# Performance work log

Measured on AMD Instinct MI355X. Metric: run time of the kernel, lower is better.

Reference implementation:

```python
import jax, jax.numpy as jnp
import numpy as np

B, L, E, H = 4, 2048, 1024, 16
D = E // H  # head_dim = 64


def setup_inputs() -> dict:
    key = jax.random.key(0)
    ks = jax.random.split(key, 8)
    s = 0.02
    return {
        "queries": jax.random.normal(ks[0], (B, L, E), jnp.float32),
        "keys": jax.random.normal(ks[1], (B, L, E), jnp.float32),
        "values": jax.random.normal(ks[2], (B, L, E), jnp.float32),
        "mask": jnp.ones((B, 1, L, L), jnp.int32),
        "Wq": jax.random.normal(ks[3], (E, E), jnp.float32) * s,
        "Wk": jax.random.normal(ks[4], (E, E), jnp.float32) * s,
        "Wv": jax.random.normal(ks[5], (E, E), jnp.float32) * s,
        "Wo": jax.random.normal(ks[6], (E, E), jnp.float32) * s,
        "bo": jax.random.normal(ks[7], (E,), jnp.float32) * s,
    }


def reference(queries, keys, values, mask, Wq, Wk, Wv, Wo, bo):
    # Linear projections (torch Linear: x @ W.T)
    q = (queries @ Wq.T).reshape(B, -1, H, D)
    k = (keys @ Wk.T).reshape(B, -1, H, D)
    v = (values @ Wv.T).reshape(B, -1, H, D)
    # scores: [B, H, Lq, Lk]
    scores = jnp.einsum("bqhd,bkhd->bhqk", q, k)
    # masked_fill BEFORE scaling, exactly as the original
    scores = jnp.where(mask == 0, jnp.float32(-1e20), scores)
    attn = jax.nn.softmax(scores / jnp.sqrt(jnp.float32(E)), axis=3)
    out = jnp.einsum("bhql,blhd->bqhd", attn, v).reshape(B, -1, H * D)
    return out @ Wo.T + bo
```

## Files before the change

kernel.cpp:

```cpp
#include <hip/hip_runtime.h>
#include <hip/hip_bf16.h>

#define B_ 4
#define L_ 2048
#define E_ 1024
#define H_ 16
#define D_ 64
#define KDIM 1024

typedef unsigned short u16;
typedef unsigned short u16x8 __attribute__((ext_vector_type(8)));
typedef short s16x8 __attribute__((ext_vector_type(8)));
typedef short s16x4 __attribute__((ext_vector_type(4)));
typedef float f32x4 __attribute__((ext_vector_type(4)));
typedef unsigned uint2v __attribute__((ext_vector_type(2)));

#define MFMA32(a, b, c) __builtin_amdgcn_mfma_f32_16x16x32_bf16(a, b, c, 0, 0, 0)

#if __has_builtin(__builtin_amdgcn_mfma_f32_16x16x16bf16_1k)
#define HAVE_M16 1
#define MFMA16(a, b, c) __builtin_amdgcn_mfma_f32_16x16x16bf16_1k(a, b, c, 0, 0, 0)
#else
#define HAVE_M16 0
#endif

__device__ inline u16 f2bf(float f) {
  union { float f; unsigned u; } v; v.f = f;
  unsigned r = v.u + 0x7fffu + ((v.u >> 16) & 1u);
  return (u16)(r >> 16);
}
__device__ inline float bf2f(u16 h) {
  union { unsigned u; float f; } v; v.u = ((unsigned)h) << 16;
  return v.f;
}
__device__ inline unsigned permrne(float hi, float lo) {
  unsigned a = __float_as_uint(lo) + 0x8000u;
  unsigned b = __float_as_uint(hi) + 0x8000u;
  return __builtin_amdgcn_perm(b, a, 0x07060302u);
}
__device__ inline float bperm_f(int byteaddr, float v) {
  return __uint_as_float((unsigned)__builtin_amdgcn_ds_bpermute(byteaddr, (int)__float_as_uint(v)));
}

typedef __attribute__((address_space(1))) const unsigned as1_u32;
typedef __attribute__((address_space(3))) unsigned as3_u32;
__device__ inline void gl_lds16(const u16* g, u16* l) {
  __builtin_amdgcn_global_load_lds((as1_u32*)g, (as3_u32*)l, 16, 0, 0);
}

__global__ __launch_bounds__(256) void detect_k(const u16* __restrict__ q, int* __restrict__ flag) {
  int tid = threadIdx.x;
  int cnt = 0;
  for (int i = tid; i < 4096; i += 256) {
    unsigned e = (q[i] >> 7) & 0xFFu;
    if (e >= 0xC0u) cnt++;
  }
  __shared__ int s[256];
  s[tid] = cnt;
  __syncthreads();
  for (int off = 128; off; off >>= 1) {
    if (tid < off) s[tid] += s[tid + off];
    __syncthreads();
  }
  if (tid == 0) *flag = (s[0] >= 16) ? 1 : 0;
}

__global__ __launch_bounds__(256) void mask_bits_k(const int* __restrict__ mask,
                                                   unsigned long long* __restrict__ bits,
                                                   unsigned* __restrict__ gflag, int words) {
  int gw = (int)((blockIdx.x * 256 + threadIdx.x) >> 6);
  int lane = threadIdx.x & 63;
  if (gw >= words) return;
  int mv = mask[(size_t)gw * 64 + lane];
  unsigned long long bal = __ballot(mv != 0);
  if (lane == 0) {
    bits[gw] = bal;
    if (bal != ~0ULL) atomicAnd(gflag, 0u);
  }
}

__global__ __launch_bounds__(256) void cvt_bf16_k(const void* __restrict__ src, u16* __restrict__ dst,
                                                  int n8, const int* __restrict__ flagp) {
  int i = blockIdx.x * 256 + threadIdx.x;
  if (i >= n8) return;
  if (*flagp) {
    const float* s = (const float*)src + (size_t)i * 8;
    f32x4 a = *(const f32x4*)s;
    f32x4 b = *(const f32x4*)(s + 4);
    u16x8 o;
#pragma unroll
    for (int j = 0; j < 4; ++j) { o[j] = f2bf(a[j]); o[4 + j] = f2bf(b[j]); }
    *((u16x8*)dst + i) = o;
  } else {
    *((u16x8*)dst + i) = *((const u16x8*)src + i);
  }
}
__global__ __launch_bounds__(256) void cvt_f32_k(const void* __restrict__ src, float* __restrict__ dst,
                                                 int n, const int* __restrict__ flagp) {
  int i = blockIdx.x * 256 + threadIdx.x;
  if (i >= n) return;
  dst[i] = (*flagp) ? ((const float*)src)[i] : bf2f(((const u16*)src)[i]);
}

__device__ inline void gemm_core(const u16* __restrict__ A, const u16* __restrict__ W,
                                 int m0, int n0, u16* AsB, u16* BsB, f32x4 (&acc)[4][4]) {
  const int tid = threadIdx.x;
  const int wave = tid >> 6, lane = tid & 63;
  const int quad = lane >> 4, l16 = lane & 15;
  const int wm = wave >> 1, wn = wave & 1;
  const int lrow = lane >> 3;
  const int lch = (lane & 7) ^ lrow;

#pragma unroll
  for (int i = 0; i < 4; ++i)
#pragma unroll
    for (int j = 0; j < 4; ++j)
#pragma unroll
      for (int u = 0; u < 4; ++u) acc[i][j][u] = 0.f;

  const u16* gA = A + (size_t)(m0 + wave * 32 + lrow) * KDIM + lch * 8;
  const u16* gB = W + (size_t)(n0 + wave * 32 + lrow) * KDIM + lch * 8;

  for (int k0 = 0; k0 < KDIM; k0 += 64) {
    __syncthreads();
#pragma unroll
    for (int i = 0; i < 4; ++i) {
      gl_lds16(gA + (size_t)i * 8 * KDIM + k0, &AsB[(wave * 32 + i * 8) * 64]);
      gl_lds16(gB + (size_t)i * 8 * KDIM + k0, &BsB[(wave * 32 + i * 8) * 64]);
    }
    __syncthreads();
#pragma unroll
    for (int ks = 0; ks < 2; ++ks) {
      s16x8 af[4], bf[4];
#pragma unroll
      for (int mt = 0; mt < 4; ++mt) {
        int row = wm * 64 + mt * 16 + l16;
        af[mt] = *(const s16x8*)&AsB[row * 64 + (((quad + 4 * ks) ^ (row & 7)) * 8)];
      }
#pragma unroll
      for (int nt = 0; nt < 4; ++nt) {
        int row = wn * 64 + nt * 16 + l16;
        bf[nt] = *(const s16x8*)&BsB[row * 64 + (((quad + 4 * ks) ^ (row & 7)) * 8)];
      }
#pragma unroll
      for (int mt = 0; mt < 4; ++mt)
#pragma unroll
        for (int nt = 0; nt < 4; ++nt)
          acc[mt][nt] = MFMA32(af[mt], bf[nt], acc[mt][nt]);
    }
  }
}

#define SCALE_Q 0.045084220f
#define MASKC  -4.508422e18f

__global__ __launch_bounds__(256) void gemm_qk_k(
    const void* __restrict__ qor, const void* __restrict__ kor,
    const void* __restrict__ wqor, const void* __restrict__ wkor,
    const u16* __restrict__ qc, const u16* __restrict__ kc,
    const u16* __restrict__ wqc, const u16* __restrict__ wkc,
    u16* __restrict__ Qp, u16* __restrict__ Kp, const int* __restrict__ flagp) {
  const int isf32 = *flagp;
  const int z = blockIdx.z;
  const u16* A = z ? (isf32 ? kc : (const u16*)kor) : (isf32 ? qc : (const u16*)qor);
  const u16* W = z ? (isf32 ? wkc : (const u16*)wkor) : (isf32 ? wqc : (const u16*)wqor);
  u16* C = z ? Kp : Qp;
  const float scale = z ? 1.0f : SCALE_Q;
  __shared__ __align__(16) u16 As[128 * 64];
  __shared__ __align__(16) u16 Bs[128 * 64];
  f32x4 acc[4][4];
  const int m0 = blockIdx.y * 128, n0 = blockIdx.x * 128;
  gemm_core(A, W, m0, n0, As, Bs, acc);

  const int lane = threadIdx.x & 63, wave = threadIdx.x >> 6;
  const int quad = lane >> 4, l16 = lane & 15;
  const int wm = wave >> 1, wn = wave & 1;
#pragma unroll
  for (int mt = 0; mt < 4; ++mt)
#pragma unroll
    for (int r = 0; r < 4; ++r) {
      int row = m0 + wm * 64 + mt * 16 + quad * 4 + r;
      int bb = row >> 11, l = row & (L_ - 1);
#pragma unroll
      for (int nt = 0; nt < 4; ++nt) {
        int col = n0 + wn * 64 + nt * 16 + l16;
        int hh = col >> 6, d = col & 63;
        C[(((size_t)bb * H_ + hh) * L_ + l) * D_ + d] = f2bf(acc[mt][nt][r] * scale);
      }
    }
}

__global__ __launch_bounds__(256) void gemm_vt_k(
    const void* __restrict__ vor, const void* __restrict__ wvor,
    const u16* __restrict__ vc, const u16* __restrict__ wvc,
    u16* __restrict__ VpT, const int* __restrict__ flagp) {
  const int isf32 = *flagp;
  const u16* A = isf32 ? wvc : (const u16*)wvor;
  const u16* W = isf32 ? vc : (const u16*)vor;
  __shared__ __align__(16) u16 As[128 * 64];
  __shared__ __align__(16) u16 Bs[128 * 64];
  f32x4 acc[4][4];
  const int m0 = blockIdx.y * 128, n0 = blockIdx.x * 128;
  gemm_core(A, W, m0, n0, As, Bs, acc);

  const int lane = threadIdx.x & 63, wave = threadIdx.x >> 6;
  const int quad = lane >> 4, l16 = lane & 15;
  const int wm = wave >> 1, wn = wave & 1;
#pragma unroll
  for (int mt = 0; mt < 4; ++mt)
#pragma unroll
    for (int r = 0; r < 4; ++r) {
      int o = m0 + wm * 64 + mt * 16 + quad * 4 + r;
      int hh = o >> 6, d = o & 63;
#pragma unroll
      for (int nt = 0; nt < 4; ++nt) {
        int t = n0 + wn * 64 + nt * 16 + l16;
        int bb = t >> 11, l = t & (L_ - 1);
        VpT[(((size_t)bb * H_ + hh) * D_ + d) * L_ + l] = f2bf(acc[mt][nt][r]);
      }
    }
}

__global__ __launch_bounds__(256) void gemm_out_k(
    const u16* __restrict__ AO, const void* __restrict__ woor, const u16* __restrict__ woc,
    const float* __restrict__ bo_f, void* __restrict__ outp, const int* __restrict__ flagp) {
  const int isf32 = *flagp;
  const u16* A = AO;
  const u16* W = isf32 ? woc : (const u16*)woor;
  __shared__ __align__(16) u16 As[128 * 64];
  __shared__ __align__(16) u16 Bs[128 * 64];
  f32x4 acc[4][4];
  const int m0 = blockIdx.y * 128, n0 = blockIdx.x * 128;
  gemm_core(A, W, m0, n0, As, Bs, acc);

  const int lane = threadIdx.x & 63, wave = threadIdx.x >> 6;
  const int quad = lane >> 4, l16 = lane & 15;
  const int wm = wave >> 1, wn = wave & 1;
#pragma unroll
  for (int mt = 0; mt < 4; ++mt)
#pragma unroll
    for (int r = 0; r < 4; ++r) {
      int row = m0 + wm * 64 + mt * 16 + quad * 4 + r;
#pragma unroll
      for (int nt = 0; nt < 4; ++nt) {
        int col = n0 + wn * 64 + nt * 16 + l16;
        float v = acc[mt][nt][r] + bo_f[col];
        if (isf32) ((float*)outp)[(size_t)row * E_ + col] = v;
        else ((u16*)outp)[(size_t)row * E_ + col] = f2bf(v);
      }
    }
}

__global__ __launch_bounds__(256) void attn_st(
    const u16* __restrict__ Qp, const u16* __restrict__ Kp, const u16* __restrict__ VpT,
    const unsigned long long* __restrict__ Mb, const unsigned* __restrict__ allonesp,
    u16* __restrict__ AO) {
  const int qt = blockIdx.x, h = blockIdx.y, b = blockIdx.z;
  const int tid = threadIdx.x;
  const int wave = tid >> 6, lane = tid & 63;
  const int quad = lane >> 4, l16 = lane & 15;
  const size_t bh = ((size_t)b * H_ + h) * (size_t)(L_ * D_);
  const int q0w = qt * 64 + wave * 16;
  const bool aone = (*allonesp) != 0u;

  __shared__ __align__(16) u16 Ks[64 * 64];
  __shared__ __align__(16) u16 Vs[64 * 64];
#if !HAVE_M16
  __shared__ __align__(16) u16 Ps[4][16 * 72];
#endif

  s16x8 bq[2];
  {
    const u16* qp = &Qp[bh + (size_t)(q0w + l16) * D_ + quad * 8];
    bq[0] = *(const s16x8*)qp;
    bq[1] = *(const s16x8*)(qp + 32);
  }

  f32x4 Oacc[4];
#pragma unroll
  for (int nt = 0; nt < 4; ++nt)
#pragma unroll
    for (int u = 0; u < 4; ++u) Oacc[nt][u] = 0.f;
  float m_i = -3.0e38f, l_i = 0.f;

  const int lrow = lane >> 3, lch = (lane & 7) ^ lrow;

  for (int kt = 0; kt < L_ / 64; ++kt) {
    const int k0 = kt * 64;
    __syncthreads();
#pragma unroll
    for (int i = 0; i < 2; ++i) {
      int row = wave * 16 + i * 8 + lrow;
      gl_lds16(&Kp[bh + (size_t)(k0 + row) * D_ + lch * 8], &Ks[(wave * 16 + i * 8) * 64]);
      gl_lds16(&VpT[bh + (size_t)row * L_ + k0 + lch * 8], &Vs[(wave * 16 + i * 8) * 64]);
    }
    __syncthreads();

    f32x4 st[4];
#pragma unroll
    for (int nt = 0; nt < 4; ++nt) {
#pragma unroll
      for (int u = 0; u < 4; ++u) st[nt][u] = 0.f;
#pragma unroll
      for (int ks = 0; ks < 2; ++ks) {
        int row = nt * 16 + l16;
        s16x8 ak = *(const s16x8*)&Ks[row * 64 + (((quad + 4 * ks) ^ (row & 7)) * 8)];
        st[nt] = MFMA32(ak, bq[ks], st[nt]);
      }
    }

    float sv[4][4];
    if (aone) {
#pragma unroll
      for (int nt = 0; nt < 4; ++nt)
#pragma unroll
        for (int r = 0; r < 4; ++r) sv[nt][r] = st[nt][r];
    } else {
      unsigned long long mb = Mb[((size_t)b * L_ + q0w + l16) * (L_ / 64) + kt];
      unsigned long long mq = mb >> (quad * 4);
#pragma unroll
      for (int nt = 0; nt < 4; ++nt)
#pragma unroll
        for (int r = 0; r < 4; ++r)
          sv[nt][r] = ((mq >> (nt * 16 + r)) & 1ULL) ? st[nt][r] : MASKC;
    }

    float mx = sv[0][0];
#pragma unroll
    for (int nt = 0; nt < 4; ++nt)
#pragma unroll
      for (int r = 0; r < 4; ++r) mx = fmaxf(mx, sv[nt][r]);
    mx = fmaxf(mx, __shfl_xor(mx, 16));
    mx = fmaxf(mx, __shfl_xor(mx, 32));
    float newm = fmaxf(m_i, mx);
    float alpha = exp2f(m_i - newm);

    float p[4][4];
    float rs = 0.f;
#pragma unroll
    for (int nt = 0; nt < 4; ++nt)
#pragma unroll
      for (int r = 0; r < 4; ++r) {
        float e = exp2f(sv[nt][r] - newm);
        p[nt][r] = e;
        rs += e;
      }
    rs += __shfl_xor(rs, 16);
    rs += __shfl_xor(rs, 32);
    l_i = l_i * alpha + rs;
    m_i = newm;

#pragma unroll
    for (int r = 0; r < 4; ++r) {
      float aO = bperm_f((quad * 4 + r) * 4, alpha);
      Oacc[0][r] *= aO; Oacc[1][r] *= aO; Oacc[2][r] *= aO; Oacc[3][r] *= aO;
    }

#if HAVE_M16
#pragma unroll
    for (int knt = 0; knt < 4; ++knt) {
      unsigned pk0 = permrne(p[knt][1], p[knt][0]);
      unsigned pk1 = permrne(p[knt][3], p[knt][2]);
      union { uint2v u; s16x4 v; } pa;
      pa.u[0] = pk0; pa.u[1] = pk1;
      const int kkb = knt * 16 + quad * 4;
      const int kch = kkb >> 3, kin = kkb & 7;
#pragma unroll
      for (int nt = 0; nt < 4; ++nt) {
        int row = nt * 16 + l16;
        s16x4 vb = *(const s16x4*)&Vs[row * 64 + ((kch ^ (row & 7)) * 8) + kin];
        Oacc[nt] = MFMA16(pa.v, vb, Oacc[nt]);
      }
    }
#else
#pragma unroll
    for (int nt = 0; nt < 4; ++nt) {
      uint2v w;
      w[0] = permrne(p[nt][1], p[nt][0]);
      w[1] = permrne(p[nt][3], p[nt][2]);
      *(uint2v*)&Ps[wave][l16 * 72 + nt * 16 + quad * 4] = w;
    }
#pragma unroll
    for (int ks = 0; ks < 2; ++ks) {
      s16x8 pa = *(const s16x8*)&Ps[wave][l16 * 72 + quad * 8 + 32 * ks];
#pragma unroll
      for (int nt = 0; nt < 4; ++nt) {
        int row = nt * 16 + l16;
        s16x8 vb = *(const s16x8*)&Vs[row * 64 + (((quad + 4 * ks) ^ (row & 7)) * 8)];
        Oacc[nt] = MFMA32(pa, vb, Oacc[nt]);
      }
    }
#endif
  }

#pragma unroll
  for (int r = 0; r < 4; ++r) {
    float lr = bperm_f((quad * 4 + r) * 4, l_i);
    float inv = 1.0f / lr;
    int row = q0w + quad * 4 + r;
#pragma unroll
    for (int nt = 0; nt < 4; ++nt) {
      int col = h * 64 + nt * 16 + l16;
      AO[((size_t)b * L_ + row) * E_ + col] = f2bf(Oacc[nt][r] * inv);
    }
  }
}

__device__ inline u16x8 load8_cvt(const void* base, size_t elem_off, int isf32) {
  if (isf32) {
    const float* p = (const float*)base + elem_off;
    f32x4 lo = *(const f32x4*)p;
    f32x4 hi = *(const f32x4*)(p + 4);
    u16x8 t;
#pragma unroll
    for (int j = 0; j < 4; ++j) { t[j] = f2bf(lo[j]); t[4 + j] = f2bf(hi[j]); }
    return t;
  } else {
    return *((const u16x8*)base + elem_off / 8);
  }
}

template <int QKV>
__global__ __launch_bounds__(256) void gemm128(
    const void* __restrict__ A0, const void* __restrict__ A1, const void* __restrict__ A2,
    const void* __restrict__ W0, const void* __restrict__ W1, const void* __restrict__ W2,
    const void* __restrict__ bias,
    void* __restrict__ C0, u16* __restrict__ C1, u16* __restrict__ C2,
    int M, int N, int Kd, const int* __restrict__ flagp) {
  const void* A = A0; const void* W = W0; void* C = C0;
  if (QKV) {
    if (blockIdx.z == 1) { A = A1; W = W1; C = C1; }
    else if (blockIdx.z == 2) { A = A2; W = W2; C = C2; }
  }
  const int isf32 = *flagp;
  const int aF32 = QKV ? isf32 : 0;
  const int tid = threadIdx.x;
  const int wave = tid >> 6, lane = tid & 63;
  const int quad = lane >> 4, l16 = lane & 15;
  const int wm = wave >> 1, wn = wave & 1;
  const int m0 = blockIdx.y * 128, n0 = blockIdx.x * 128;
  __shared__ u16 As[128 * 32];
  __shared__ u16 Bs[128 * 32];
  f32x4 acc[4][4];
#pragma unroll
  for (int i = 0; i < 4; ++i)
#pragma unroll
    for (int j = 0; j < 4; ++j)
#pragma unroll
      for (int u = 0; u < 4; ++u) acc[i][j][u] = 0.f;
  const int row_s = tid >> 2;
  const int cb_s = tid & 3;
  for (int k0 = 0; k0 < Kd; k0 += 32) {
    __syncthreads();
#pragma unroll
    for (int rr = 0; rr < 2; ++rr) {
      int row = rr * 64 + row_s;
      int sw = (cb_s ^ ((row >> 1) & 3)) * 8;
      *(u16x8*)&As[row * 32 + sw] = load8_cvt(A, (size_t)(m0 + row) * Kd + k0 + cb_s * 8, aF32);
      *(u16x8*)&Bs[row * 32 + sw] = load8_cvt(W, (size_t)(n0 + row) * Kd + k0 + cb_s * 8, isf32);
    }
    __syncthreads();
    s16x8 af[4], bfv[4];
#pragma unroll
    for (int mt = 0; mt < 4; ++mt) {
      int row = wm * 64 + mt * 16 + l16;
      af[mt] = *(const s16x8*)&As[row * 32 + (quad ^ ((row >> 1) & 3)) * 8];
    }
#pragma unroll
    for (int nt = 0; nt < 4; ++nt) {
      int row = wn * 64 + nt * 16 + l16;
      bfv[nt] = *(const s16x8*)&Bs[row * 32 + (quad ^ ((row >> 1) & 3)) * 8];
    }
#pragma unroll
    for (int mt = 0; mt < 4; ++mt)
#pragma unroll
      for (int nt = 0; nt < 4; ++nt)
        acc[mt][nt] = MFMA32(af[mt], bfv[nt], acc[mt][nt]);
  }
#pragma unroll
  for (int mt = 0; mt < 4; ++mt)
#pragma unroll
    for (int r = 0; r < 4; ++r) {
      int row = m0 + wm * 64 + mt * 16 + quad * 4 + r;
#pragma unroll
      for (int nt = 0; nt < 4; ++nt) {
        int col = n0 + wn * 64 + nt * 16 + l16;
        float v = acc[mt][nt][r];
        if (!QKV) {
          v += isf32 ? ((const float*)bias)[col] : bf2f(((const u16*)bias)[col]);
          if (isf32) ((float*)C)[(size_t)row * N + col] = v;
          else ((u16*)C)[(size_t)row * N + col] = f2bf(v);
        } else {
          int bb = row >> 11, l = row & (L_ - 1);
          int hh = col >> 6, d = col & 63;
          ((u16*)C)[(((size_t)bb * H_ + hh) * L_ + l) * D_ + d] = f2bf(v);
        }
      }
    }
}

__global__ __launch_bounds__(256) void attn64(const u16* __restrict__ Qp, const u16* __restrict__ Kp,
                                              const u16* __restrict__ Vp,
                                              const unsigned long long* __restrict__ Mb,
                                              u16* __restrict__ AO) {
  const int qt = blockIdx.x, h = blockIdx.y, b = blockIdx.z;
  const int tid = threadIdx.x;
  const int wave = tid >> 6, lane = tid & 63;
  const int quad = lane >> 4, l16 = lane & 15;
  const size_t bh = ((size_t)b * H_ + h) * (size_t)(L_ * D_);
  const int q0 = qt * 64;
  __shared__ u16 Ksl[64 * 72];
  __shared__ u16 Vtl[64 * 72];
  __shared__ u16 Psl[4][16 * 72];
  s16x8 aq[2];
  {
    int qrow = q0 + wave * 16 + l16;
#pragma unroll
    for (int ks = 0; ks < 2; ++ks)
      aq[ks] = *(const s16x8*)&Qp[bh + (size_t)qrow * D_ + quad * 8 + 32 * ks];
  }
  f32x4 Oacc[4];
#pragma unroll
  for (int nt = 0; nt < 4; ++nt)
#pragma unroll
    for (int u = 0; u < 4; ++u) Oacc[nt][u] = 0.f;
  float m_i[4], l_i[4];
#pragma unroll
  for (int r = 0; r < 4; ++r) { m_i[r] = -3.0e38f; l_i[r] = 0.f; }
  const float invs = 0.03125f;
  const float LOG2E = 1.44269504088896f;
  for (int kt = 0; kt < L_ / 64; ++kt) {
    const int k0 = kt * 64;
    __syncthreads();
#pragma unroll
    for (int rr = 0; rr < 2; ++rr) {
      int row = rr * 32 + (tid >> 3);
      int col = (tid & 7) * 8;
      *(u16x8*)&Ksl[row * 72 + col] = *(const u16x8*)&Kp[bh + (size_t)(k0 + row) * D_ + col];
    }
    {
      int d0 = wave * 16;
#pragma unroll
      for (int half = 0; half < 2; ++half) {
        u16x8 tv = *(const u16x8*)&Vp[bh + (size_t)(k0 + lane) * D_ + d0 + half * 8];
#pragma unroll
        for (int j = 0; j < 8; ++j) Vtl[(d0 + half * 8 + j) * 72 + lane] = tv[j];
      }
    }
    __syncthreads();
    f32x4 sacc[4];
#pragma unroll
    for (int nt = 0; nt < 4; ++nt) {
#pragma unroll
      for (int u = 0; u < 4; ++u) sacc[nt][u] = 0.f;
#pragma unroll
      for (int ks = 0; ks < 2; ++ks) {
        s16x8 bfr = *(const s16x8*)&Ksl[(nt * 16 + l16) * 72 + quad * 8 + 32 * ks];
        sacc[nt] = MFMA32(aq[ks], bfr, sacc[nt]);
      }
    }
    float sv[4][4], alph[4];
#pragma unroll
    for (int r = 0; r < 4; ++r) {
      int row = q0 + wave * 16 + quad * 4 + r;
      unsigned long long mb = Mb[(size_t)(b * L_ + row) * (L_ / 64) + kt];
#pragma unroll
      for (int nt = 0; nt < 4; ++nt) {
        float s = sacc[nt][r] * invs;
        if (!((mb >> (nt * 16 + l16)) & 1ULL)) s = -3.125e18f;
        sv[nt][r] = s;
      }
      float mx = fmaxf(fmaxf(sv[0][r], sv[1][r]), fmaxf(sv[2][r], sv[3][r]));
      mx = fmaxf(mx, __shfl_xor(mx, 1));
      mx = fmaxf(mx, __shfl_xor(mx, 2));
      mx = fmaxf(mx, __shfl_xor(mx, 4));
      mx = fmaxf(mx, __shfl_xor(mx, 8));
      float newm = fmaxf(m_i[r], mx);
      float alpha = exp2f((m_i[r] - newm) * LOG2E);
      float rs = 0.f;
#pragma unroll
      for (int nt = 0; nt < 4; ++nt) {
        float pp = exp2f((sv[nt][r] - newm) * LOG2E);
        rs += pp;
        Psl[wave][(quad * 4 + r) * 72 + nt * 16 + l16] = f2bf(pp);
      }
      rs += __shfl_xor(rs, 1);
      rs += __shfl_xor(rs, 2);
      rs += __shfl_xor(rs, 4);
      rs += __shfl_xor(rs, 8);
      l_i[r] = l_i[r] * alpha + rs;
      m_i[r] = newm;
      alph[r] = alpha;
    }
#pragma unroll
    for (int nt = 0; nt < 4; ++nt)
#pragma unroll
      for (int r = 0; r < 4; ++r) Oacc[nt][r] *= alph[r];
#pragma unroll
    for (int ks = 0; ks < 2; ++ks) {
      s16x8 pa = *(const s16x8*)&Psl[wave][l16 * 72 + quad * 8 + 32 * ks];
#pragma unroll
      for (int nt = 0; nt < 4; ++nt) {
        s16x8 vb = *(const s16x8*)&Vtl[(nt * 16 + l16) * 72 + quad * 8 + 32 * ks];
        Oacc[nt] = MFMA32(pa, vb, Oacc[nt]);
      }
    }
  }
#pragma unroll
  for (int nt = 0; nt < 4; ++nt)
#pragma unroll
    for (int r = 0; r < 4; ++r) {
      int row = q0 + wave * 16 + quad * 4 + r;
      int col = h * 64 + nt * 16 + l16;
      AO[((size_t)b * L_ + row) * E_ + col] = f2bf(Oacc[nt][r] / l_i[r]);
    }
}

extern "C" void kernel_launch(void* const* d_in, const int* in_sizes, int n_in,
                              void* d_out, int out_size, void* d_ws, size_t ws_size,
                              hipStream_t stream) {
  const void* queries = d_in[0];
  const void* keys = d_in[1];
  const void* values = d_in[2];
  const int* mask = (const int*)d_in[3];
  const void* Wq = d_in[4];
  const void* Wk = d_in[5];
  const void* Wv = d_in[6];
  const void* Wo = d_in[7];
  const void* bo = d_in[8];

  char* ws = (char*)d_ws;
  const int words = B_ * L_ * (L_ / 64);
  const size_t NEED = 111153408;

  if (ws_size >= NEED) {
    const size_t SZQ = (size_t)B_ * L_ * E_ * 2;
    const size_t SZW = (size_t)E_ * E_ * 2;
    u16* qc = (u16*)(ws + 0);
    u16* kc = (u16*)(ws + SZQ);
    u16* vc = (u16*)(ws + 2 * SZQ);
    u16* wqc = (u16*)(ws + 3 * SZQ);
    u16* wkc = (u16*)(ws + 3 * SZQ + SZW);
    u16* wvc = (u16*)(ws + 3 * SZQ + 2 * SZW);
    u16* woc = (u16*)(ws + 3 * SZQ + 3 * SZW);
    float* bo_f = (float*)(ws + 3 * SZQ + 4 * SZW);
    char* p2 = ws + 3 * SZQ + 4 * SZW + 4096;
    u16* Qp = (u16*)(p2);
    u16* Kp = (u16*)(p2 + SZQ);
    u16* VpT = (u16*)(p2 + 2 * SZQ);
    unsigned long long* Mb = (unsigned long long*)(p2 + 3 * SZQ);
    char* pf = p2 + 3 * SZQ + (size_t)words * 8;
    int* flag = (int*)pf;
    unsigned* gflag = (unsigned*)(pf + 4);
    u16* AO = qc;

    hipLaunchKernelGGL(detect_k, dim3(1), dim3(256), 0, stream, (const u16*)queries, flag);
    hipMemsetAsync(gflag, 1, 4, stream);
    hipLaunchKernelGGL(mask_bits_k, dim3(words / 4), dim3(256), 0, stream, mask, Mb, gflag, words);

    int n8q = (B_ * L_ * E_) / 8, n8w = (E_ * E_) / 8;
    hipLaunchKernelGGL(cvt_bf16_k, dim3(n8q / 256), dim3(256), 0, stream, queries, qc, n8q, flag);
    hipLaunchKernelGGL(cvt_bf16_k, dim3(n8q / 256), dim3(256), 0, stream, keys, kc, n8q, flag);
    hipLaunchKernelGGL(cvt_bf16_k, dim3(n8q / 256), dim3(256), 0, stream, values, vc, n8q, flag);
    hipLaunchKernelGGL(cvt_bf16_k, dim3(n8w / 256), dim3(256), 0, stream, Wq, wqc, n8w, flag);
    hipLaunchKernelGGL(cvt_bf16_k, dim3(n8w / 256), dim3(256), 0, stream, Wk, wkc, n8w, flag);
    hipLaunchKernelGGL(cvt_bf16_k, dim3(n8w / 256), dim3(256), 0, stream, Wv, wvc, n8w, flag);
    hipLaunchKernelGGL(cvt_bf16_k, dim3(n8w / 256), dim3(256), 0, stream, Wo, woc, n8w, flag);
    hipLaunchKernelGGL(cvt_f32_k, dim3(E_ / 256), dim3(256), 0, stream, bo, bo_f, E_, flag);

    hipLaunchKernelGGL(gemm_qk_k, dim3(E_ / 128, (B_ * L_) / 128, 2), dim3(256), 0, stream,
                       queries, keys, Wq, Wk, qc, kc, wqc, wkc, Qp, Kp, flag);
    hipLaunchKernelGGL(gemm_vt_k, dim3((B_ * L_) / 128, E_ / 128, 1), dim3(256), 0, stream,
                       values, Wv, vc, wvc, VpT, flag);
    hipLaunchKernelGGL(attn_st, dim3(L_ / 64, H_, B_), dim3(256), 0, stream,
                       Qp, Kp, VpT, Mb, gflag, AO);
    hipLaunchKernelGGL(gemm_out_k, dim3(E_ / 128, (B_ * L_) / 128, 1), dim3(256), 0, stream,
                       AO, Wo, woc, bo_f, d_out, flag);
  } else {
    const size_t SEG = (size_t)B_ * H_ * L_ * D_ * sizeof(u16);
    u16* Qp = (u16*)(ws);
    u16* Kp = (u16*)(ws + SEG);
    u16* Vp = (u16*)(ws + 2 * SEG);
    u16* AO = (u16*)(ws + 3 * SEG);
    int* flag = (int*)(ws + 4 * SEG);
    unsigned* gflag = (unsigned*)(ws + 4 * SEG + 8);
    unsigned long long* Mb = (unsigned long long*)(ws + 4 * SEG + 256);

    hipLaunchKernelGGL(detect_k, dim3(1), dim3(256), 0, stream, (const u16*)queries, flag);
    hipMemsetAsync(gflag, 1, 4, stream);
    hipLaunchKernelGGL(mask_bits_k, dim3(words / 4), dim3(256), 0, stream, mask, Mb, gflag, words);
    dim3 g1(E_ / 128, (B_ * L_) / 128, 3);
    hipLaunchKernelGGL((gemm128<1>), g1, dim3(256), 0, stream,
                       queries, keys, values, Wq, Wk, Wv, (const void*)nullptr,
                       (void*)Qp, Kp, Vp, B_ * L_, E_, E_, flag);
    hipLaunchKernelGGL(attn64, dim3(L_ / 64, H_, B_), dim3(256), 0, stream, Qp, Kp, Vp, Mb, AO);
    dim3 g2(E_ / 128, (B_ * L_) / 128, 1);
    hipLaunchKernelGGL((gemm128<0>), g2, dim3(256), 0, stream,
                       (const void*)AO, (const void*)nullptr, (const void*)nullptr,
                       Wo, (const void*)nullptr, (const void*)nullptr, bo,
                       d_out, (u16*)nullptr, (u16*)nullptr, B_ * L_, E_, E_, flag);
  }
}
```

Before: 486.3 us.

## Fuse conversion and projection launches, widen attention K tile to 128 with fp16 PV

Merges the eight per-tensor conversion launches into one kernel, and the Q/K and V projection GEMMs into a single three-slice launch. V is now stored in fp16. The attention kernel processes 128 keys per iteration with a new swizzled V layout and uses fp16 MFMA for P·V, with probabilities packed by cvt_pkrtz and raw exp2 intrinsics. The aims are to cut launch overhead and halve the number of attention loop iterations and syncs. The costs are more LDS and registers per block and fp16 range and precision for V and P.

```diff
diff --git a/kernel.cpp b/kernel.cpp
--- a/kernel.cpp
+++ b/kernel.cpp
@@ -11,17 +11,20 @@
 typedef unsigned short u16;
 typedef unsigned short u16x8 __attribute__((ext_vector_type(8)));
 typedef short s16x8 __attribute__((ext_vector_type(8)));
-typedef short s16x4 __attribute__((ext_vector_type(4)));
 typedef float f32x4 __attribute__((ext_vector_type(4)));
 typedef unsigned uint2v __attribute__((ext_vector_type(2)));
+typedef __fp16 h16x2 __attribute__((ext_vector_type(2)));
+typedef __fp16 h16x4 __attribute__((ext_vector_type(4)));
+typedef __fp16 h16x8 __attribute__((ext_vector_type(8)));
 
 #define MFMA32(a, b, c) __builtin_amdgcn_mfma_f32_16x16x32_bf16(a, b, c, 0, 0, 0)
-
-#if __has_builtin(__builtin_amdgcn_mfma_f32_16x16x16bf16_1k)
-#define HAVE_M16 1
-#define MFMA16(a, b, c) __builtin_amdgcn_mfma_f32_16x16x16bf16_1k(a, b, c, 0, 0, 0)
+#define MFMA32F(a, b, c) __builtin_amdgcn_mfma_f32_16x16x32_f16(a, b, c, 0, 0, 0)
+
+#if __has_builtin(__builtin_amdgcn_mfma_f32_16x16x16f16)
+#define HAVE_F16K16 1
+#define MFMA16F(a, b, c) __builtin_amdgcn_mfma_f32_16x16x16f16(a, b, c, 0, 0, 0)
 #else
-#define HAVE_M16 0
+#define HAVE_F16K16 0
 #endif
 
 __device__ inline u16 f2bf(float f) {
@@ -33,13 +36,12 @@
   union { unsigned u; float f; } v; v.u = ((unsigned)h) << 16;
   return v.f;
 }
-__device__ inline unsigned permrne(float hi, float lo) {
-  unsigned a = __float_as_uint(lo) + 0x8000u;
-  unsigned b = __float_as_uint(hi) + 0x8000u;
-  return __builtin_amdgcn_perm(b, a, 0x07060302u);
-}
 __device__ inline float bperm_f(int byteaddr, float v) {
   return __uint_as_float((unsigned)__builtin_amdgcn_ds_bpermute(byteaddr, (int)__float_as_uint(v)));
+}
+__device__ inline u16 f2h_bits(float f) {
+  union { __fp16 h; u16 u; } c; c.h = (__fp16)f;
+  return c.u;
 }
 
 typedef __attribute__((address_space(1))) const unsigned as1_u32;
@@ -47,6 +49,9 @@
 __device__ inline void gl_lds16(const u16* g, u16* l) {
   __builtin_amdgcn_global_load_lds((as1_u32*)g, (as3_u32*)l, 16, 0, 0);
 }
+
+#define SCALE_Q 0.045084220f
+#define MASKC  -4.508422e18f
 
 __global__ __launch_bounds__(256) void detect_k(const u16* __restrict__ q, int* __restrict__ flag) {
   int tid = threadIdx.x;
@@ -79,27 +84,56 @@
   }
 }
 
-__global__ __launch_bounds__(256) void cvt_bf16_k(const void* __restrict__ src, u16* __restrict__ dst,
-                                                  int n8, const int* __restrict__ flagp) {
-  int i = blockIdx.x * 256 + threadIdx.x;
-  if (i >= n8) return;
-  if (*flagp) {
-    const float* s = (const float*)src + (size_t)i * 8;
-    f32x4 a = *(const f32x4*)s;
-    f32x4 b = *(const f32x4*)(s + 4);
-    u16x8 o;
-#pragma unroll
-    for (int j = 0; j < 4; ++j) { o[j] = f2bf(a[j]); o[4 + j] = f2bf(b[j]); }
-    *((u16x8*)dst + i) = o;
+#define CH_ACT (1 << 20)
+#define CH_W (1 << 17)
+#define CH_TOT (128 + 3 * CH_ACT + 4 * CH_W)
+__global__ __launch_bounds__(256) void cvt_all_k(
+    const void* __restrict__ q, const void* __restrict__ k, const void* __restrict__ v,
+    const void* __restrict__ wq, const void* __restrict__ wk, const void* __restrict__ wv,
+    const void* __restrict__ wo, const void* __restrict__ bo,
+    u16* __restrict__ qc, u16* __restrict__ kc, u16* __restrict__ vc,
+    u16* __restrict__ wqc, u16* __restrict__ wkc, u16* __restrict__ wvc, u16* __restrict__ woc,
+    float* __restrict__ bo_f, const int* __restrict__ flagp) {
+  int c = blockIdx.x * 256 + threadIdx.x;
+  if (c >= CH_TOT) return;
+  const int isf32 = *flagp;
+  if (c < 128) {
+    if (isf32) {
+      f32x4 a = *((const f32x4*)bo + c * 2);
+      f32x4 b2 = *((const f32x4*)bo + c * 2 + 1);
+      *((f32x4*)bo_f + c * 2) = a;
+      *((f32x4*)bo_f + c * 2 + 1) = b2;
+    } else {
+      const u16* s = (const u16*)bo + c * 8;
+#pragma unroll
+      for (int j = 0; j < 8; ++j) bo_f[c * 8 + j] = bf2f(s[j]);
+    }
+    return;
+  }
+  if (!isf32) return;
+  c -= 128;
+  const void* src;
+  u16* dst;
+  size_t off;
+  if (c < 3 * CH_ACT) {
+    int t = c >> 20;
+    off = (size_t)(c & (CH_ACT - 1));
+    src = t == 0 ? q : (t == 1 ? k : v);
+    dst = t == 0 ? qc : (t == 1 ? kc : vc);
   } else {
-    *((u16x8*)dst + i) = *((const u16x8*)src + i);
-  }
-}
-__global__ __launch_bounds__(256) void cvt_f32_k(const void* __restrict__ src, float* __restrict__ dst,
-                                                 int n, const int* __restrict__ flagp) {
-  int i = blockIdx.x * 256 + threadIdx.x;
-  if (i >= n) return;
-  dst[i] = (*flagp) ? ((const float*)src)[i] : bf2f(((const u16*)src)[i]);
+    int d = c - 3 * CH_ACT;
+    int t = d >> 17;
+    off = (size_t)(d & (CH_W - 1));
+    src = t == 0 ? wq : (t == 1 ? wk : (t == 2 ? wv : wo));
+    dst = t == 0 ? wqc : (t == 1 ? wkc : (t == 2 ? wvc : woc));
+  }
+  const float* s = (const float*)src + off * 8;
+  f32x4 a = *(const f32x4*)s;
+  f32x4 b2 = *(const f32x4*)(s + 4);
+  u16x8 o;
+#pragma unroll
+  for (int j = 0; j < 4; ++j) { o[j] = f2bf(a[j]); o[4 + j] = f2bf(b2[j]); }
+  *((u16x8*)dst + off) = o;
 }
 
 __device__ inline void gemm_core(const u16* __restrict__ A, const u16* __restrict__ W,
@@ -151,87 +185,74 @@
   }
 }
 
-#define SCALE_Q 0.045084220f
-#define MASKC  -4.508422e18f
-
-__global__ __launch_bounds__(256) void gemm_qk_k(
-    const void* __restrict__ qor, const void* __restrict__ kor,
-    const void* __restrict__ wqor, const void* __restrict__ wkor,
-    const u16* __restrict__ qc, const u16* __restrict__ kc,
-    const u16* __restrict__ wqc, const u16* __restrict__ wkc,
-    u16* __restrict__ Qp, u16* __restrict__ Kp, const int* __restrict__ flagp) {
+__global__ __launch_bounds__(256) void gemm_proj_k(
+    const void* __restrict__ qor, const void* __restrict__ kor, const void* __restrict__ vor,
+    const void* __restrict__ wqor, const void* __restrict__ wkor, const void* __restrict__ wvor,
+    const u16* __restrict__ qc, const u16* __restrict__ kc, const u16* __restrict__ vc,
+    const u16* __restrict__ wqc, const u16* __restrict__ wkc, const u16* __restrict__ wvc,
+    u16* __restrict__ Qp, u16* __restrict__ Kp, u16* __restrict__ VpT,
+    const int* __restrict__ flagp) {
   const int isf32 = *flagp;
   const int z = blockIdx.z;
-  const u16* A = z ? (isf32 ? kc : (const u16*)kor) : (isf32 ? qc : (const u16*)qor);
-  const u16* W = z ? (isf32 ? wkc : (const u16*)wkor) : (isf32 ? wqc : (const u16*)wqor);
-  u16* C = z ? Kp : Qp;
-  const float scale = z ? 1.0f : SCALE_Q;
   __shared__ __align__(16) u16 As[128 * 64];
   __shared__ __align__(16) u16 Bs[128 * 64];
   f32x4 acc[4][4];
-  const int m0 = blockIdx.y * 128, n0 = blockIdx.x * 128;
-  gemm_core(A, W, m0, n0, As, Bs, acc);
 
   const int lane = threadIdx.x & 63, wave = threadIdx.x >> 6;
   const int quad = lane >> 4, l16 = lane & 15;
   const int wm = wave >> 1, wn = wave & 1;
-#pragma unroll
-  for (int mt = 0; mt < 4; ++mt)
-#pragma unroll
-    for (int r = 0; r < 4; ++r) {
-      int row = m0 + wm * 64 + mt * 16 + quad * 4 + r;
-      int bb = row >> 11, l = row & (L_ - 1);
-#pragma unroll
-      for (int nt = 0; nt < 4; ++nt) {
-        int col = n0 + wn * 64 + nt * 16 + l16;
-        int hh = col >> 6, d = col & 63;
-        C[(((size_t)bb * H_ + hh) * L_ + l) * D_ + d] = f2bf(acc[mt][nt][r] * scale);
-      }
-    }
-}
-
-__global__ __launch_bounds__(256) void gemm_vt_k(
-    const void* __restrict__ vor, const void* __restrict__ wvor,
-    const u16* __restrict__ vc, const u16* __restrict__ wvc,
-    u16* __restrict__ VpT, const int* __restrict__ flagp) {
-  const int isf32 = *flagp;
-  const u16* A = isf32 ? wvc : (const u16*)wvor;
-  const u16* W = isf32 ? vc : (const u16*)vor;
-  __shared__ __align__(16) u16 As[128 * 64];
-  __shared__ __align__(16) u16 Bs[128 * 64];
-  f32x4 acc[4][4];
-  const int m0 = blockIdx.y * 128, n0 = blockIdx.x * 128;
-  gemm_core(A, W, m0, n0, As, Bs, acc);
-
-  const int lane = threadIdx.x & 63, wave = threadIdx.x >> 6;
-  const int quad = lane >> 4, l16 = lane & 15;
-  const int wm = wave >> 1, wn = wave & 1;
-#pragma unroll
-  for (int mt = 0; mt < 4; ++mt)
-#pragma unroll
-    for (int r = 0; r < 4; ++r) {
-      int o = m0 + wm * 64 + mt * 16 + quad * 4 + r;
-      int hh = o >> 6, d = o & 63;
-#pragma unroll
-      for (int nt = 0; nt < 4; ++nt) {
-        int t = n0 + wn * 64 + nt * 16 + l16;
-        int bb = t >> 11, l = t & (L_ - 1);
-        VpT[(((size_t)bb * H_ + hh) * D_ + d) * L_ + l] = f2bf(acc[mt][nt][r]);
-      }
-    }
+
+  if (z < 2) {
+    const u16* A = z ? (isf32 ? kc : (const u16*)kor) : (isf32 ? qc : (const u16*)qor);
+    const u16* W = z ? (isf32 ? wkc : (const u16*)wkor) : (isf32 ? wqc : (const u16*)wqor);
+    u16* C = z ? Kp : Qp;
+    const float scale = z ? 1.0f : SCALE_Q;
+    const int m0 = blockIdx.y * 128, n0 = blockIdx.x * 128;
+    gemm_core(A, W, m0, n0, As, Bs, acc);
+#pragma unroll
+    for (int mt = 0; mt < 4; ++mt)
+#pragma unroll
+      for (int r = 0; r < 4; ++r) {
+        int row = m0 + wm * 64 + mt * 16 + quad * 4 + r;
+        int bb = row >> 11, l = row & (L_ - 1);
+#pragma unroll
+        for (int nt = 0; nt < 4; ++nt) {
+          int col = n0 + wn * 64 + nt * 16 + l16;
+          int hh = col >> 6, d = col & 63;
+          C[(((size_t)bb * H_ + hh) * L_ + l) * D_ + d] = f2bf(acc[mt][nt][r] * scale);
+        }
+      }
+  } else {
+    const u16* A = isf32 ? wvc : (const u16*)wvor;
+    const u16* W = isf32 ? vc : (const u16*)vor;
+    const int m0 = blockIdx.x * 128, n0 = blockIdx.y * 128;
+    gemm_core(A, W, m0, n0, As, Bs, acc);
+#pragma unroll
+    for (int mt = 0; mt < 4; ++mt)
+#pragma unroll
+      for (int r = 0; r < 4; ++r) {
+        int o = m0 + wm * 64 + mt * 16 + quad * 4 + r;
+        int hh = o >> 6, d = o & 63;
+#pragma unroll
+        for (int nt = 0; nt < 4; ++nt) {
+          int t = n0 + wn * 64 + nt * 16 + l16;
+          int bb = t >> 11, l = t & (L_ - 1);
+          VpT[(((size_t)bb * H_ + hh) * D_ + d) * L_ + l] = f2h_bits(acc[mt][nt][r]);
+        }
+      }
+  }
 }
 
 __global__ __launch_bounds__(256) void gemm_out_k(
     const u16* __restrict__ AO, const void* __restrict__ woor, const u16* __restrict__ woc,
     const float* __restrict__ bo_f, void* __restrict__ outp, const int* __restrict__ flagp) {
   const int isf32 = *flagp;
-  const u16* A = AO;
   const u16* W = isf32 ? woc : (const u16*)woor;
   __shared__ __align__(16) u16 As[128 * 64];
   __shared__ __align__(16) u16 Bs[128 * 64];
   f32x4 acc[4][4];
   const int m0 = blockIdx.y * 128, n0 = blockIdx.x * 128;
-  gemm_core(A, W, m0, n0, As, Bs, acc);
+  gemm_core(AO, W, m0, n0, As, Bs, acc);
 
   const int lane = threadIdx.x & 63, wave = threadIdx.x >> 6;
   const int quad = lane >> 4, l16 = lane & 15;
@@ -251,7 +272,7 @@
     }
 }
 
-__global__ __launch_bounds__(256) void attn_st(
+__global__ __launch_bounds__(256) void attn_st2(
     const u16* __restrict__ Qp, const u16* __restrict__ Kp, const u16* __restrict__ VpT,
     const unsigned long long* __restrict__ Mb, const unsigned* __restrict__ allonesp,
     u16* __restrict__ AO) {
@@ -263,10 +284,10 @@
   const int q0w = qt * 64 + wave * 16;
   const bool aone = (*allonesp) != 0u;
 
-  __shared__ __align__(16) u16 Ks[64 * 64];
-  __shared__ __align__(16) u16 Vs[64 * 64];
-#if !HAVE_M16
-  __shared__ __align__(16) u16 Ps[4][16 * 72];
+  __shared__ __align__(16) u16 Ks[128 * 64];
+  __shared__ __align__(16) u16 Vs[64 * 128];
+#if !HAVE_F16K16
+  __shared__ __align__(16) u16 Ps[4][16 * 136];
 #endif
 
   s16x8 bq[2];
@@ -284,67 +305,78 @@
   float m_i = -3.0e38f, l_i = 0.f;
 
   const int lrow = lane >> 3, lch = (lane & 7) ^ lrow;
-
-  for (int kt = 0; kt < L_ / 64; ++kt) {
-    const int k0 = kt * 64;
-    __syncthreads();
-#pragma unroll
-    for (int i = 0; i < 2; ++i) {
-      int row = wave * 16 + i * 8 + lrow;
-      gl_lds16(&Kp[bh + (size_t)(k0 + row) * D_ + lch * 8], &Ks[(wave * 16 + i * 8) * 64]);
-      gl_lds16(&VpT[bh + (size_t)row * L_ + k0 + lch * 8], &Vs[(wave * 16 + i * 8) * 64]);
-    }
-    __syncthreads();
-
-    f32x4 st[4];
-#pragma unroll
-    for (int nt = 0; nt < 4; ++nt) {
-#pragma unroll
-      for (int u = 0; u < 4; ++u) st[nt][u] = 0.f;
-#pragma unroll
-      for (int ks = 0; ks < 2; ++ks) {
-        int row = nt * 16 + l16;
-        s16x8 ak = *(const s16x8*)&Ks[row * 64 + (((quad + 4 * ks) ^ (row & 7)) * 8)];
-        st[nt] = MFMA32(ak, bq[ks], st[nt]);
-      }
-    }
-
-    float sv[4][4];
-    if (aone) {
-#pragma unroll
-      for (int nt = 0; nt < 4; ++nt)
-#pragma unroll
-        for (int r = 0; r < 4; ++r) sv[nt][r] = st[nt][r];
-    } else {
-      unsigned long long mb = Mb[((size_t)b * L_ + q0w + l16) * (L_ / 64) + kt];
-      unsigned long long mq = mb >> (quad * 4);
-#pragma unroll
-      for (int nt = 0; nt < 4; ++nt)
-#pragma unroll
-        for (int r = 0; r < 4; ++r)
-          sv[nt][r] = ((mq >> (nt * 16 + r)) & 1ULL) ? st[nt][r] : MASKC;
-    }
-
-    float mx = sv[0][0];
-#pragma unroll
-    for (int nt = 0; nt < 4; ++nt)
-#pragma unroll
-      for (int r = 0; r < 4; ++r) mx = fmaxf(mx, sv[nt][r]);
+  const int vd_sub = lane >> 4;
+  const int vchp = lane & 15;
+
+  for (int kt = 0; kt < L_ / 128; ++kt) {
+    const int k0 = kt * 128;
+    __syncthreads();
+#pragma unroll
+    for (int i = 0; i < 4; ++i) {
+      int krow = (wave * 4 + i) * 8 + lrow;
+      gl_lds16(&Kp[bh + (size_t)(k0 + krow) * D_ + lch * 8], &Ks[(wave * 4 + i) * 512]);
+    }
+#pragma unroll
+    for (int i = 0; i < 4; ++i) {
+      int d = wave * 16 + i * 4 + vd_sub;
+      int c = vchp ^ (i * 4 + vd_sub);
+      gl_lds16(&VpT[bh + (size_t)d * L_ + k0 + c * 8], &Vs[(wave * 16 + i * 4) * 128]);
+    }
+    __syncthreads();
+
+    float s[8][4];
+#pragma unroll
+    for (int h2 = 0; h2 < 2; ++h2)
+#pragma unroll
+      for (int nt = 0; nt < 4; ++nt) {
+        f32x4 a = {0.f, 0.f, 0.f, 0.f};
+        int row = h2 * 64 + nt * 16 + l16;
+#pragma unroll
+        for (int ks = 0; ks < 2; ++ks) {
+          s16x8 ak = *(const s16x8*)&Ks[row * 64 + (((quad + 4 * ks) ^ (row & 7)) * 8)];
+          a = MFMA32(ak, bq[ks], a);
+        }
+#pragma unroll
+        for (int r = 0; r < 4; ++r) s[h2 * 4 + nt][r] = a[r];
+      }
+
+    if (!aone) {
+      const unsigned long long* mrow = &Mb[((size_t)b * L_ + q0w + l16) * (L_ / 64) + kt * 2];
+      unsigned long long mb0 = mrow[0] >> (quad * 4);
+      unsigned long long mb1 = mrow[1] >> (quad * 4);
+#pragma unroll
+      for (int h2 = 0; h2 < 2; ++h2) {
+        unsigned long long mb = h2 ? mb1 : mb0;
+#pragma unroll
+        for (int nt = 0; nt < 4; ++nt)
+#pragma unroll
+          for (int r = 0; r < 4; ++r)
+            if (!((mb >> (nt * 16 + r)) & 1ULL)) s[h2 * 4 + nt][r] = MASKC;
+      }
+    }
+
+    float mx = s[0][0];
+#pragma unroll
+    for (int knt = 0; knt < 8; ++knt)
+#pragma unroll
+      for (int r = 0; r < 4; ++r) mx = fmaxf(mx, s[knt][r]);
     mx = fmaxf(mx, __shfl_xor(mx, 16));
     mx = fmaxf(mx, __shfl_xor(mx, 32));
     float newm = fmaxf(m_i, mx);
-    float alpha = exp2f(m_i - newm);
-
-    float p[4][4];
+    float alpha = __builtin_amdgcn_exp2f(m_i - newm);
+
     float rs = 0.f;
 #pragma unroll
-    for (int nt = 0; nt < 4; ++nt)
+    for (int knt = 0; knt < 8; ++knt) {
+      float t0 = 0.f;
 #pragma unroll
       for (int r = 0; r < 4; ++r) {
-        float e = exp2f(sv[nt][r] - newm);
-        p[nt][r] = e;
-        rs += e;
-      }
+        float e = __builtin_amdgcn_exp2f(s[knt][r] - newm);
+        s[knt][r] = e;
+        t0 += e;
+      }
+      rs += t0;
+    }
     rs += __shfl_xor(rs, 16);
     rs += __shfl_xor(rs, 32);
     l_i = l_i * alpha + rs;
@@ -356,38 +388,38 @@
       Oacc[0][r] *= aO; Oacc[1][r] *= aO; Oacc[2][r] *= aO; Oacc[3][r] *= aO;
     }
 
-#if HAVE_M16
-#pragma unroll
-    for (int knt = 0; knt < 4; ++knt) {
-      unsigned pk0 = permrne(p[knt][1], p[knt][0]);
-      unsigned pk1 = permrne(p[knt][3], p[knt][2]);
-      union { uint2v u; s16x4 v; } pa;
-      pa.u[0] = pk0; pa.u[1] = pk1;
-      const int kkb = knt * 16 + quad * 4;
-      const int kch = kkb >> 3, kin = kkb & 7;
-#pragma unroll
-      for (int nt = 0; nt < 4; ++nt) {
-        int row = nt * 16 + l16;
-        s16x4 vb = *(const s16x4*)&Vs[row * 64 + ((kch ^ (row & 7)) * 8) + kin];
-        Oacc[nt] = MFMA16(pa.v, vb, Oacc[nt]);
+#if HAVE_F16K16
+#pragma unroll
+    for (int knt = 0; knt < 8; ++knt) {
+      union { h16x2 h2[2]; h16x4 v4; } pu;
+      pu.h2[0] = __builtin_amdgcn_cvt_pkrtz(s[knt][0], s[knt][1]);
+      pu.h2[1] = __builtin_amdgcn_cvt_pkrtz(s[knt][2], s[knt][3]);
+      const int cbase = knt * 2 + (quad >> 1);
+      const int sub = (quad & 1) * 4;
+#pragma unroll
+      for (int nt = 0; nt < 4; ++nt) {
+        int d = nt * 16 + l16;
+        const __fp16* vp = (const __fp16*)&Vs[d * 128 + ((cbase ^ (d & 15)) * 8) + sub];
+        Oacc[nt] = MFMA16F(pu.v4, *(const h16x4*)vp, Oacc[nt]);
       }
     }
 #else
 #pragma unroll
-    for (int nt = 0; nt < 4; ++nt) {
-      uint2v w;
-      w[0] = permrne(p[nt][1], p[nt][0]);
-      w[1] = permrne(p[nt][3], p[nt][2]);
-      *(uint2v*)&Ps[wave][l16 * 72 + nt * 16 + quad * 4] = w;
-    }
-#pragma unroll
-    for (int ks = 0; ks < 2; ++ks) {
-      s16x8 pa = *(const s16x8*)&Ps[wave][l16 * 72 + quad * 8 + 32 * ks];
-#pragma unroll
-      for (int nt = 0; nt < 4; ++nt) {
-        int row = nt * 16 + l16;
-        s16x8 vb = *(const s16x8*)&Vs[row * 64 + (((quad + 4 * ks) ^ (row & 7)) * 8)];
-        Oacc[nt] = MFMA32(pa, vb, Oacc[nt]);
+    for (int knt = 0; knt < 8; ++knt) {
+      union { h16x2 h2[2]; uint2v u; } pu;
+      pu.h2[0] = __builtin_amdgcn_cvt_pkrtz(s[knt][0], s[knt][1]);
+      pu.h2[1] = __builtin_amdgcn_cvt_pkrtz(s[knt][2], s[knt][3]);
+      *(uint2v*)&Ps[wave][l16 * 136 + knt * 16 + quad * 4] = pu.u;
+    }
+#pragma unroll
+    for (int ks = 0; ks < 4; ++ks) {
+      h16x8 pa = *(const h16x8*)&Ps[wave][l16 * 136 + ks * 32 + quad * 8];
+#pragma unroll
+      for (int nt = 0; nt < 4; ++nt) {
+        int d = nt * 16 + l16;
+        int c = (ks * 4 + quad) ^ (d & 15);
+        h16x8 vb = *(const h16x8*)&Vs[d * 128 + c * 8];
+        Oacc[nt] = MFMA32F(pa, vb, Oacc[nt]);
       }
     }
 #endif
@@ -655,24 +687,15 @@
     u16* AO = qc;
 
     hipLaunchKernelGGL(detect_k, dim3(1), dim3(256), 0, stream, (const u16*)queries, flag);
-    hipMemsetAsync(gflag, 1, 4, stream);
+    (void)hipMemsetAsync(gflag, 1, 4, stream);
     hipLaunchKernelGGL(mask_bits_k, dim3(words / 4), dim3(256), 0, stream, mask, Mb, gflag, words);
-
-    int n8q = (B_ * L_ * E_) / 8, n8w = (E_ * E_) / 8;
-    hipLaunchKernelGGL(cvt_bf16_k, dim3(n8q / 256), dim3(256), 0, stream, queries, qc, n8q, flag);
-    hipLaunchKernelGGL(cvt_bf16_k, dim3(n8q / 256), dim3(256), 0, stream, keys, kc, n8q, flag);
-    hipLaunchKernelGGL(cvt_bf16_k, dim3(n8q / 256), dim3(256), 0, stream, values, vc, n8q, flag);
-    hipLaunchKernelGGL(cvt_bf16_k, dim3(n8w / 256), dim3(256), 0, stream, Wq, wqc, n8w, flag);
-    hipLaunchKernelGGL(cvt_bf16_k, dim3(n8w / 256), dim3(256), 0, stream, Wk, wkc, n8w, flag);
-    hipLaunchKernelGGL(cvt_bf16_k, dim3(n8w / 256), dim3(256), 0, stream, Wv, wvc, n8w, flag);
-    hipLaunchKernelGGL(cvt_bf16_k, dim3(n8w / 256), dim3(256), 0, stream, Wo, woc, n8w, flag);
-    hipLaunchKernelGGL(cvt_f32_k, dim3(E_ / 256), dim3(256), 0, stream, bo, bo_f, E_, flag);
-
-    hipLaunchKernelGGL(gemm_qk_k, dim3(E_ / 128, (B_ * L_) / 128, 2), dim3(256), 0, stream,
-                       queries, keys, Wq, Wk, qc, kc, wqc, wkc, Qp, Kp, flag);
-    hipLaunchKernelGGL(gemm_vt_k, dim3((B_ * L_) / 128, E_ / 128, 1), dim3(256), 0, stream,
-                       values, Wv, vc, wvc, VpT, flag);
-    hipLaunchKernelGGL(attn_st, dim3(L_ / 64, H_, B_), dim3(256), 0, stream,
+    hipLaunchKernelGGL(cvt_all_k, dim3((CH_TOT + 255) / 256), dim3(256), 0, stream,
+                       queries, keys, values, Wq, Wk, Wv, Wo, bo,
+                       qc, kc, vc, wqc, wkc, wvc, woc, bo_f, flag);
+    hipLaunchKernelGGL(gemm_proj_k, dim3(E_ / 128, (B_ * L_) / 128, 3), dim3(256), 0, stream,
+                       queries, keys, values, Wq, Wk, Wv,
+                       qc, kc, vc, wqc, wkc, wvc, Qp, Kp, VpT, flag);
+    hipLaunchKernelGGL(attn_st2, dim3(L_ / 64, H_, B_), dim3(256), 0, stream,
                        Qp, Kp, VpT, Mb, gflag, AO);
     hipLaunchKernelGGL(gemm_out_k, dim3(E_ / 128, (B_ * L_) / 128, 1), dim3(256), 0, stream,
                        AO, Wo, woc, bo_f, d_out, flag);
@@ -687,7 +710,7 @@
     unsigned long long* Mb = (unsigned long long*)(ws + 4 * SEG + 256);
 
     hipLaunchKernelGGL(detect_k, dim3(1), dim3(256), 0, stream, (const u16*)queries, flag);
-    hipMemsetAsync(gflag, 1, 4, stream);
+    (void)hipMemsetAsync(gflag, 1, 4, stream);
     hipLaunchKernelGGL(mask_bits_k, dim3(words / 4), dim3(256), 0, stream, mask, Mb, gflag, words);
     dim3 g1(E_ / 128, (B_ * L_) / 128, 3);
     hipLaunchKernelGGL((gemm128<1>), g1, dim3(256), 0, stream,
```

Measured after the change: 444.5 us. -8.6%, faster.
